# Optimization experiments

Hardware: AMD Instinct MI355X
Metric: run time of the kernel (lower is better)

## Reference

```python
import jax, jax.numpy as jnp
import numpy as np

B, D = 64, 65536   # batch, num default boxes
NEG_POS = 3        # negative:positive mining ratio (init arg)


def _bce_with_logits(x, t):
    # numerically stable elementwise BCE-with-logits (matches torch)
    return jnp.maximum(x, 0.0) - x * t + jnp.log1p(jnp.exp(-jnp.abs(x)))


def _smooth_l1(d):
    ad = jnp.abs(d)
    return jnp.where(ad < 1.0, 0.5 * d * d, ad - 0.5)


def setup_inputs() -> dict:
    key = jax.random.key(0)
    k1, k2, k3, k4 = jax.random.split(key, 4)
    loc_data = jax.random.normal(k1, (B, D, 4), dtype=jnp.float32)
    conf_data = jax.random.normal(k2, (B, D, 1), dtype=jnp.float32)
    loc_t = jax.random.normal(k3, (B, D, 4), dtype=jnp.float32)
    conf_t = (jax.random.uniform(k4, (B, D)) < 0.02).astype(jnp.int32)
    return {"loc_data": loc_data, "conf_data": conf_data,
            "loc_t": loc_t, "conf_t": conf_t}


def reference(loc_data, conf_data, loc_t, conf_t):
    pos = conf_t > 0                                  # [B, D]
    num_pos = pos.sum(axis=1, keepdims=True)          # [B, 1]

    # ---- localization loss: smooth-L1 mean over positive box coords ----
    pf = pos[:, :, None].astype(loc_data.dtype)       # [B, D, 1]
    sl1 = _smooth_l1(loc_data - loc_t) * pf           # [B, D, 4]
    n_loc_elems = pf.sum() * 4.0                      # masked-gather -> mean
    loss_l = sl1.sum() / n_loc_elems

    # ---- confidence loss with hard negative mining ----
    logits = conf_data[:, :, 0]                       # [B, D]
    bce = _bce_with_logits(logits, conf_t.astype(logits.dtype))
    bce_neg = jnp.where(pos, 0.0, bce)                # zero-out positives
    # double argsort -> per-row rank of each element's loss (descending)
    loss_idx = jnp.argsort(-bce_neg, axis=1)          # [B, D]
    idx_rank = jnp.argsort(loss_idx, axis=1)          # [B, D]
    num_neg = jnp.minimum(num_pos * NEG_POS, D)       # [B, 1]
    neg = idx_rank < num_neg                          # top-k hardest negatives
    sel = (pos | neg).astype(logits.dtype)            # [B, D]
    loss_c = (bce * sel).sum() / sel.sum()            # mean over selected

    N = num_pos.sum().astype(logits.dtype)
    return (loss_l / N, loss_c / N)
```

## Files before the change

### kernel.cpp

```cpp
#include <hip/hip_runtime.h>
#include <stdint.h>


#define B_ 64
#define D_ 65536
#define NEGPOS 3
#define BPR 16
#define NBLK (B_ * BPR)
#define CHUNK (D_ / BPR)
#define XC 1.25f
#define CAPC 16384
#define NREG 32
#define HBINS 4096
#define XRANGE 5.0f
#define CJCAP 1024

#define OFF_SL1P     0
#define OFF_BCEP     8192
#define OFF_NP       16384
#define OFF_CC       20480
#define OFF_NEGSUM   24576
#define OFF_KSEL     25088
#define OFF_CAND     32768

__device__ __forceinline__ float softplus_f(float x) {
    return fmaxf(x, 0.0f) + log1pf(expf(-fabsf(x)));
}

__device__ __forceinline__ unsigned sortkey(float x) {
    unsigned u = __float_as_uint(x);
    return (u & 0x80000000u) ? ~u : (u | 0x80000000u);
}
__device__ __forceinline__ float unsortkey(unsigned s) {
    unsigned u = (s & 0x80000000u) ? (s & 0x7FFFFFFFu) : ~s;
    return __uint_as_float(u);
}

__device__ __forceinline__ int bin_of_x(float x) {
    int b = (int)((x - XC) * ((float)HBINS / XRANGE));
    return max(0, min(HBINS - 1, b));
}

__device__ __forceinline__ float smooth_l1_4(float4 a, float4 b) {
    float s = 0.0f, d, ad;
    d = a.x - b.x; ad = fabsf(d); s += (ad < 1.0f) ? 0.5f * d * d : ad - 0.5f;
    d = a.y - b.y; ad = fabsf(d); s += (ad < 1.0f) ? 0.5f * d * d : ad - 0.5f;
    d = a.z - b.z; ad = fabsf(d); s += (ad < 1.0f) ? 0.5f * d * d : ad - 0.5f;
    d = a.w - b.w; ad = fabsf(d); s += (ad < 1.0f) ? 0.5f * d * d : ad - 0.5f;
    return s;
}

__device__ __forceinline__ double wredD(double v) {
#pragma unroll
    for (int o = 32; o > 0; o >>= 1) v += __shfl_down(v, o, 64);
    return v;
}
__device__ __forceinline__ int wredI(int v) {
#pragma unroll
    for (int o = 32; o > 0; o >>= 1) v += __shfl_down(v, o, 64);
    return v;
}

__global__ void __launch_bounds__(256)
mbl_k1(const float4* __restrict__ loc4, const float* __restrict__ conf,
       const float4* __restrict__ loct4, const int* __restrict__ conft,
       unsigned char* __restrict__ ws)
{
    __shared__ float lcand[CHUNK];
    __shared__ unsigned short lpos[CHUNK];
    __shared__ unsigned wtot[4];
    __shared__ double wr[8];

    const int block = blockIdx.x;
    const int base = block * CHUNK;
    const float4* c4 = (const float4*)(conf + base);
    const int4*   t4 = (const int4*)(conft + base);
    const int lane = threadIdx.x & 63, wid = threadIdx.x >> 6;

    float4 xv[4]; int4 tv[4];
#pragma unroll
    for (int it = 0; it < 4; it++) {
        const int g = threadIdx.x + it * 256;
        xv[it] = c4[g];
        tv[it] = t4[g];
    }

    double bcep = 0.0;
    unsigned cntc = 0, cntp = 0;
#pragma unroll
    for (int it = 0; it < 4; it++) {
#pragma unroll
        for (int c = 0; c < 4; c++) {
            float x = (c == 0) ? xv[it].x : (c == 1) ? xv[it].y : (c == 2) ? xv[it].z : xv[it].w;
            int   t = (c == 0) ? tv[it].x : (c == 1) ? tv[it].y : (c == 2) ? tv[it].z : tv[it].w;
            if (t > 0) { cntp++; bcep += (double)(softplus_f(x) - x); }
            else if (x >= XC) cntc++;
        }
    }

    unsigned pk = (cntc << 16) | cntp;
    unsigned incl = pk;
#pragma unroll
    for (int o = 1; o < 64; o <<= 1) {
        unsigned v = __shfl_up(incl, o, 64);
        if (lane >= o) incl += v;
    }
    unsigned excl = incl - pk;
    if (lane == 63) wtot[wid] = incl;
    __syncthreads();
    unsigned wbase = 0;
    for (int w = 0; w < wid; w++) wbase += wtot[w];
    const unsigned tot = wtot[0] + wtot[1] + wtot[2] + wtot[3];
    const unsigned totc = tot >> 16, totp = tot & 0xFFFFu;
    unsigned offc = (excl >> 16) + (wbase >> 16);
    unsigned offp = (excl & 0xFFFFu) + (wbase & 0xFFFFu);

#pragma unroll
    for (int it = 0; it < 4; it++) {
#pragma unroll
        for (int c = 0; c < 4; c++) {
            float x = (c == 0) ? xv[it].x : (c == 1) ? xv[it].y : (c == 2) ? xv[it].z : xv[it].w;
            int   t = (c == 0) ? tv[it].x : (c == 1) ? tv[it].y : (c == 2) ? tv[it].z : tv[it].w;
            const int li = (threadIdx.x + it * 256) * 4 + c;
            if (t > 0) lpos[offp++] = (unsigned short)li;
            else if (x >= XC) lcand[offc++] = x;
        }
    }
    __syncthreads();

    float* seg = (float*)(ws + OFF_CAND) + (size_t)block * CHUNK;
    for (unsigned i = threadIdx.x; i < totc; i += 256) seg[i] = lcand[i];

    double sl1 = 0.0;
    for (unsigned i = threadIdx.x; i < totp; i += 256) {
        const int e = base + (int)lpos[i];
        sl1 += (double)smooth_l1_4(loc4[e], loct4[e]);
    }

    double s1 = wredD(sl1), s2 = wredD(bcep);
    if (lane == 0) { wr[wid] = s1; wr[4 + wid] = s2; }
    __syncthreads();
    if (threadIdx.x == 0) {
        ((double*)(ws + OFF_SL1P))[block] = wr[0] + wr[1] + wr[2] + wr[3];
        ((double*)(ws + OFF_BCEP))[block] = wr[4] + wr[5] + wr[6] + wr[7];
        ((unsigned*)(ws + OFF_NP))[block] = totp;
        ((unsigned*)(ws + OFF_CC))[block] = totc;
    }
}

__device__ __forceinline__ int blockSumI(int v, int* sh) {
    int w = wredI(v);
    const int lane = threadIdx.x & 63, wid = threadIdx.x >> 6;
    __syncthreads();
    if (lane == 0) sh[wid] = w;
    __syncthreads();
    return sh[0] + sh[1] + sh[2] + sh[3];
}

__global__ void __launch_bounds__(256)
mbl_ksel(const float* __restrict__ conf, const int* __restrict__ conft,
         unsigned char* __restrict__ ws)
{
    __shared__ unsigned segoff[BPR + 1];
    __shared__ unsigned hist[HBINS];
    __shared__ unsigned part[256];
    __shared__ unsigned ubuf[CJCAP];
    __shared__ unsigned shJ, shRemJ, shCj, shT;
    __shared__ int shI[4];
    __shared__ double wr[4];

    const int row = blockIdx.x;
    const unsigned* cc = (const unsigned*)(ws + OFF_CC) + row * BPR;
    const unsigned* npb = (const unsigned*)(ws + OFF_NP) + row * BPR;

    if (threadIdx.x == 0) {
        unsigned o = 0;
        int np = 0;
#pragma unroll
        for (int s = 0; s < BPR; s++) { segoff[s] = o; o += cc[s]; np += (int)npb[s]; }
        segoff[BPR] = o;
        shI[0] = np;
    }
    __syncthreads();
    const int np = shI[0];
    const unsigned n = segoff[BPR];
    long long k = (long long)np * NEGPOS;
    if (k > D_) k = D_;
    long long negs = (long long)D_ - np;
    if (k > negs) k = negs;
    if (threadIdx.x == 0) ((int*)(ws + OFF_KSEL))[row] = (int)k;
    if (k <= 0) {
        if (threadIdx.x == 0) ((double*)(ws + OFF_NEGSUM))[row] = 0.0;
        return;
    }
    __syncthreads();

    const bool fb = ((long long)n < k) || (n > (unsigned)(NREG * 256)) ||
                    (n > (unsigned)CAPC);
    const float* cand = (const float*)(ws + OFF_CAND);
    const float* rowc = conf + row * D_;
    const int*   rowt = conft + row * D_;
    const int lane = threadIdx.x & 63, wid = threadIdx.x >> 6;
    unsigned Tkey;
    int rem;

    if (!fb) {
        unsigned keys[NREG];
#pragma unroll
        for (int j = 0; j < NREG; j++) {
            const unsigned g = (unsigned)(j * 256) + threadIdx.x;
            unsigned key = 0u;
            if (g < n) {
                int s = 0;
#pragma unroll
                for (int st = 8; st > 0; st >>= 1)
                    if (s + st <= BPR && segoff[s + st] <= g) s += st;
                const unsigned idx = g - segoff[s];
                key = sortkey(cand[(size_t)(row * BPR + s) * CHUNK + idx]);
            }
            keys[j] = key;
        }

        for (int i = threadIdx.x; i < HBINS; i += 256) hist[i] = 0;
        __syncthreads();
#pragma unroll
        for (int j = 0; j < NREG; j++)
            if (keys[j]) atomicAdd(&hist[bin_of_x(unsortkey(keys[j]))], 1u);
        __syncthreads();

        {
            unsigned s = 0; const int b0 = threadIdx.x * 16;
#pragma unroll
            for (int i = 0; i < 16; i++) s += hist[b0 + i];
            part[threadIdx.x] = s;
        }
        __syncthreads();
        if (threadIdx.x == 0) {
            long long cum = 0; unsigned J = 0, remJ = 0;
            for (int t = 255; t >= 0; t--) {
                if (cum + (long long)part[t] >= k) {
                    for (int b = t * 16 + 15; b >= t * 16; b--) {
                        cum += hist[b];
                        if (cum >= k) {
                            J = (unsigned)b;
                            remJ = (unsigned)(k - (cum - (long long)hist[b]));
                            break;
                        }
                    }
                    break;
                }
                cum += part[t];
            }
            shJ = J; shRemJ = remJ; shCj = 0;
        }
        __syncthreads();
        const unsigned J = shJ, remJ = shRemJ;

#pragma unroll
        for (int j = 0; j < NREG; j++) {
            if (keys[j] && (unsigned)bin_of_x(unsortkey(keys[j])) == J) {
                unsigned p = atomicAdd(&shCj, 1u);
                if (p < CJCAP) ubuf[p] = keys[j];
            }
        }
        __syncthreads();
        const unsigned cj = shCj;

        if (cj <= CJCAP) {
            for (unsigned i = threadIdx.x; i < cj; i += 256) {
                const unsigned ki = ubuf[i];
                unsigned gt = 0, ge = 0;
                for (unsigned l = 0; l < cj; l++) {
                    const unsigned kl = ubuf[l];
                    gt += (kl > ki) ? 1u : 0u;
                    ge += (kl >= ki) ? 1u : 0u;
                }
                if (gt < remJ && ge >= remJ) shT = ki;
            }
            __syncthreads();
            Tkey = shT;
        } else {
            unsigned lo = 0u, hi = 0xFFFFFFFFu;
            for (int it = 0; it < 32; it++) {
                const unsigned mid = lo + ((hi - lo) >> 1);
                int c = 0;
#pragma unroll
                for (int j = 0; j < NREG; j++) c += (keys[j] > mid) ? 1 : 0;
                const int tot = blockSumI(c, shI);
                if ((long long)tot >= k) lo = mid; else hi = mid;
            }
            Tkey = hi;
        }

        int c = 0;
        double acc = 0.0;
#pragma unroll
        for (int j = 0; j < NREG; j++) {
            if (keys[j] > Tkey) { c++; acc += (double)softplus_f(unsortkey(keys[j])); }
        }
        const int tot = blockSumI(c, shI);
        rem = (int)(k - (long long)tot);
        double t = wredD(acc);
        if (lane == 0) wr[wid] = t;
        __syncthreads();
        if (threadIdx.x == 0)
            ((double*)(ws + OFF_NEGSUM))[row] =
                wr[0] + wr[1] + wr[2] + wr[3] +
                (double)rem * (double)softplus_f(unsortkey(Tkey));
    } else {
        unsigned lo = 0u, hi = 0xFFFFFFFFu;
        for (int it = 0; it < 32; it++) {
            const unsigned mid = lo + ((hi - lo) >> 1);
            int c = 0;
            for (int i = threadIdx.x; i < D_; i += 256)
                if (rowt[i] <= 0 && sortkey(rowc[i]) > mid) c++;
            const int tot = blockSumI(c, shI);
            if ((long long)tot >= k) lo = mid; else hi = mid;
        }
        Tkey = hi;
        int c = 0;
        double acc = 0.0;
        for (int i = threadIdx.x; i < D_; i += 256) {
            if (rowt[i] <= 0) {
                float x = rowc[i];
                if (sortkey(x) > Tkey) { c++; acc += (double)softplus_f(x); }
            }
        }
        rem = (int)(k - (long long)blockSumI(c, shI));
        double t = wredD(acc);
        if (lane == 0) wr[wid] = t;
        __syncthreads();
        if (threadIdx.x == 0)
            ((double*)(ws + OFF_NEGSUM))[row] =
                wr[0] + wr[1] + wr[2] + wr[3] +
                (double)rem * (double)softplus_f(unsortkey(Tkey));
    }
}

__global__ void __launch_bounds__(256)
mbl_k5(unsigned char* __restrict__ ws, float* __restrict__ out)
{
    __shared__ double wrA[4], wrB[4], wrC[4];
    __shared__ int shN[4], shK[4];
    const double* sl1p = (const double*)(ws + OFF_SL1P);
    const double* bcep = (const double*)(ws + OFF_BCEP);
    const unsigned* npb = (const unsigned*)(ws + OFF_NP);
    const int* ksel = (const int*)(ws + OFF_KSEL);
    const double* ns = (const double*)(ws + OFF_NEGSUM);

    double a = 0.0, b = 0.0, c = 0.0;
    int n = 0, kk = 0;
    for (int i = threadIdx.x; i < NBLK; i += 256) {
        a += sl1p[i]; b += bcep[i]; n += (int)npb[i];
    }
    if (threadIdx.x < 64) { kk = ksel[threadIdx.x]; c = ns[threadIdx.x]; }

    double ra = wredD(a), rb = wredD(b), rc = wredD(c);
    int rn = wredI(n), rk = wredI(kk);
    const int lane = threadIdx.x & 63, wid = threadIdx.x >> 6;
    if (lane == 0) { wrA[wid] = ra; wrB[wid] = rb; wrC[wid] = rc; shN[wid] = rn; shK[wid] = rk; }
    __syncthreads();
    if (threadIdx.x == 0) {
        double SL1 = wrA[0] + wrA[1] + wrA[2] + wrA[3];
        double BCE = wrB[0] + wrB[1] + wrB[2] + wrB[3];
        double NSUM = wrC[0] + wrC[1] + wrC[2] + wrC[3];
        double Np = (double)(shN[0] + shN[1] + shN[2] + shN[3]);
        double Kt = (double)(shK[0] + shK[1] + shK[2] + shK[3]);
        double out0 = (Np > 0.0) ? (SL1 / (4.0 * Np)) / Np : 0.0;
        double denom = Np + Kt;
        double out1 = (Np > 0.0 && denom > 0.0) ? ((BCE + NSUM) / denom) / Np : 0.0;
        out[0] = (float)out0;
        out[1] = (float)out1;
    }
}

extern "C" void kernel_launch(void* const* d_in, const int* in_sizes, int n_in,
                              void* d_out, int out_size, void* d_ws, size_t ws_size,
                              hipStream_t stream)
{
    const float4* loc4  = (const float4*)d_in[0];
    const float*  conf  = (const float*)d_in[1];
    const float4* loct4 = (const float4*)d_in[2];
    const int*    conft = (const int*)d_in[3];
    unsigned char* ws = (unsigned char*)d_ws;
    float* out = (float*)d_out;

    mbl_k1<<<dim3(NBLK), dim3(256), 0, stream>>>(loc4, conf, loct4, conft, ws);
    mbl_ksel<<<dim3(B_), dim3(256), 0, stream>>>(conf, conft, ws);
    mbl_k5<<<dim3(1), dim3(256), 0, stream>>>(ws, out);
}
```

Baseline: 195.2 us.

## Stage candidates in LDS and parallelize histogram threshold search in ksel

The top-k selection kernel now copies each row's candidate logits into a shared-memory buffer with coalesced per-segment loads, replacing the 32 register keys per thread that needed a per-element segment binary search. The serial single-thread scan over the histogram is replaced by a wave-shuffle suffix scan, so every thread checks its own 16-bin group for the threshold bin. Threshold comparisons work on floats directly instead of converted sort keys. The goal is lower register pressure and less serial work, at the cost of 32KB more LDS, which may reduce occupancy.

```diff
diff --git a/kernel.cpp b/kernel.cpp
--- a/kernel.cpp
+++ b/kernel.cpp
@@ -9,8 +9,7 @@
 #define NBLK (B_ * BPR)
 #define CHUNK (D_ / BPR)
 #define XC 1.25f
-#define CAPC 16384
-#define NREG 32
+#define LCAP 8192
 #define HBINS 4096
 #define XRANGE 5.0f
 #define CJCAP 1024
@@ -25,15 +24,6 @@
 
 __device__ __forceinline__ float softplus_f(float x) {
     return fmaxf(x, 0.0f) + log1pf(expf(-fabsf(x)));
-}
-
-__device__ __forceinline__ unsigned sortkey(float x) {
-    unsigned u = __float_as_uint(x);
-    return (u & 0x80000000u) ? ~u : (u | 0x80000000u);
-}
-__device__ __forceinline__ float unsortkey(unsigned s) {
-    unsigned u = (s & 0x80000000u) ? (s & 0x7FFFFFFFu) : ~s;
-    return __uint_as_float(u);
 }
 
 __device__ __forceinline__ int bin_of_x(float x) {
@@ -161,28 +151,42 @@
 mbl_ksel(const float* __restrict__ conf, const int* __restrict__ conft,
          unsigned char* __restrict__ ws)
 {
-    __shared__ unsigned segoff[BPR + 1];
+    __shared__ float lval[LCAP];
     __shared__ unsigned hist[HBINS];
     __shared__ unsigned part[256];
     __shared__ unsigned ubuf[CJCAP];
-    __shared__ unsigned shJ, shRemJ, shCj, shT;
+    __shared__ unsigned segoff[BPR + 1];
+    __shared__ unsigned scc[BPR];
+    __shared__ unsigned wsuf[4];
+    __shared__ unsigned shJ, shRemJ, shCj, shNP;
+    __shared__ float shXT;
     __shared__ int shI[4];
     __shared__ double wr[4];
 
     const int row = blockIdx.x;
     const unsigned* cc = (const unsigned*)(ws + OFF_CC) + row * BPR;
     const unsigned* npb = (const unsigned*)(ws + OFF_NP) + row * BPR;
-
-    if (threadIdx.x == 0) {
-        unsigned o = 0;
-        int np = 0;
-#pragma unroll
-        for (int s = 0; s < BPR; s++) { segoff[s] = o; o += cc[s]; np += (int)npb[s]; }
-        segoff[BPR] = o;
-        shI[0] = np;
-    }
-    __syncthreads();
-    const int np = shI[0];
+    const int lane = threadIdx.x & 63, wid = threadIdx.x >> 6;
+
+    if (wid == 0) {
+        unsigned c = (lane < BPR) ? cc[lane] : 0u;
+        unsigned p = (lane < BPR) ? npb[lane] : 0u;
+        unsigned inc = c;
+#pragma unroll
+        for (int o = 1; o < BPR; o <<= 1) {
+            unsigned v = __shfl_up(inc, o, 64);
+            if (lane >= o) inc += v;
+        }
+        unsigned ptot = p;
+#pragma unroll
+        for (int o = 1; o < BPR; o <<= 1) ptot += __shfl_down(ptot, o, 64);
+        if (lane < BPR) { segoff[lane] = inc - c; scc[lane] = c; }
+        if (lane == BPR - 1) segoff[BPR] = inc;
+        if (lane == 0) { shNP = ptot; shCj = 0; }
+    }
+    __syncthreads();
+
+    const int np = (int)shNP;
     const unsigned n = segoff[BPR];
     long long k = (long long)np * NEGPOS;
     if (k > D_) k = D_;
@@ -193,39 +197,25 @@
         if (threadIdx.x == 0) ((double*)(ws + OFF_NEGSUM))[row] = 0.0;
         return;
     }
-    __syncthreads();
-
-    const bool fb = ((long long)n < k) || (n > (unsigned)(NREG * 256)) ||
-                    (n > (unsigned)CAPC);
+
     const float* cand = (const float*)(ws + OFF_CAND);
     const float* rowc = conf + row * D_;
     const int*   rowt = conft + row * D_;
-    const int lane = threadIdx.x & 63, wid = threadIdx.x >> 6;
-    unsigned Tkey;
+    const bool fb = ((long long)n < k) || (n > (unsigned)LCAP);
+    float xT;
     int rem;
 
     if (!fb) {
-        unsigned keys[NREG];
-#pragma unroll
-        for (int j = 0; j < NREG; j++) {
-            const unsigned g = (unsigned)(j * 256) + threadIdx.x;
-            unsigned key = 0u;
-            if (g < n) {
-                int s = 0;
-#pragma unroll
-                for (int st = 8; st > 0; st >>= 1)
-                    if (s + st <= BPR && segoff[s + st] <= g) s += st;
-                const unsigned idx = g - segoff[s];
-                key = sortkey(cand[(size_t)(row * BPR + s) * CHUNK + idx]);
-            }
-            keys[j] = key;
-        }
-
+        {
+            const int s = threadIdx.x >> 4, li = threadIdx.x & 15;
+            const float* gseg = cand + (size_t)(row * BPR + s) * CHUNK;
+            const unsigned cs = scc[s], d0 = segoff[s];
+            for (unsigned i = li; i < cs; i += 16) lval[d0 + i] = gseg[i];
+        }
         for (int i = threadIdx.x; i < HBINS; i += 256) hist[i] = 0;
         __syncthreads();
-#pragma unroll
-        for (int j = 0; j < NREG; j++)
-            if (keys[j]) atomicAdd(&hist[bin_of_x(unsortkey(keys[j]))], 1u);
+        for (unsigned i = threadIdx.x; i < n; i += 256)
+            atomicAdd(&hist[bin_of_x(lval[i])], 1u);
         __syncthreads();
 
         {
@@ -233,34 +223,38 @@
 #pragma unroll
             for (int i = 0; i < 16; i++) s += hist[b0 + i];
             part[threadIdx.x] = s;
-        }
-        __syncthreads();
-        if (threadIdx.x == 0) {
-            long long cum = 0; unsigned J = 0, remJ = 0;
-            for (int t = 255; t >= 0; t--) {
-                if (cum + (long long)part[t] >= k) {
-                    for (int b = t * 16 + 15; b >= t * 16; b--) {
-                        cum += hist[b];
-                        if (cum >= k) {
-                            J = (unsigned)b;
-                            remJ = (unsigned)(k - (cum - (long long)hist[b]));
-                            break;
-                        }
+            unsigned suf = s;
+#pragma unroll
+            for (int o = 1; o < 64; o <<= 1) {
+                unsigned v = __shfl_down(suf, o, 64);
+                if (lane + o < 64) suf += v;
+            }
+            if (lane == 0) wsuf[wid] = suf;
+            __syncthreads();
+            unsigned add = 0;
+            for (int w = wid + 1; w < 4; w++) add += wsuf[w];
+            suf += add;
+            const unsigned sufx = suf - s;
+            if ((long long)sufx < k && (long long)suf >= k) {
+                long long cum = sufx;
+                for (int b = threadIdx.x * 16 + 15; b >= threadIdx.x * 16; b--) {
+                    cum += hist[b];
+                    if (cum >= k) {
+                        shJ = (unsigned)b;
+                        shRemJ = (unsigned)(k - (cum - (long long)hist[b]));
+                        break;
                     }
-                    break;
                 }
-                cum += part[t];
-            }
-            shJ = J; shRemJ = remJ; shCj = 0;
+            }
         }
         __syncthreads();
         const unsigned J = shJ, remJ = shRemJ;
 
-#pragma unroll
-        for (int j = 0; j < NREG; j++) {
-            if (keys[j] && (unsigned)bin_of_x(unsortkey(keys[j])) == J) {
+        for (unsigned i = threadIdx.x; i < n; i += 256) {
+            float x = lval[i];
+            if ((unsigned)bin_of_x(x) == J) {
                 unsigned p = atomicAdd(&shCj, 1u);
-                if (p < CJCAP) ubuf[p] = keys[j];
+                if (p < CJCAP) ubuf[p] = __float_as_uint(x);
             }
         }
         __syncthreads();
@@ -268,35 +262,36 @@
 
         if (cj <= CJCAP) {
             for (unsigned i = threadIdx.x; i < cj; i += 256) {
-                const unsigned ki = ubuf[i];
+                const float xi = __uint_as_float(ubuf[i]);
                 unsigned gt = 0, ge = 0;
                 for (unsigned l = 0; l < cj; l++) {
-                    const unsigned kl = ubuf[l];
-                    gt += (kl > ki) ? 1u : 0u;
-                    ge += (kl >= ki) ? 1u : 0u;
+                    const float xl = __uint_as_float(ubuf[l]);
+                    gt += (xl > xi) ? 1u : 0u;
+                    ge += (xl >= xi) ? 1u : 0u;
                 }
-                if (gt < remJ && ge >= remJ) shT = ki;
+                if (gt < remJ && ge >= remJ) shXT = xi;
             }
             __syncthreads();
-            Tkey = shT;
+            xT = shXT;
         } else {
-            unsigned lo = 0u, hi = 0xFFFFFFFFu;
-            for (int it = 0; it < 32; it++) {
-                const unsigned mid = lo + ((hi - lo) >> 1);
+            float flo = XC - 1.0f, fhi = XC + XRANGE + 1.0f;
+            for (int it = 0; it < 40; it++) {
+                const float mid = 0.5f * (flo + fhi);
                 int c = 0;
-#pragma unroll
-                for (int j = 0; j < NREG; j++) c += (keys[j] > mid) ? 1 : 0;
+                for (unsigned i = threadIdx.x; i < n; i += 256)
+                    if (lval[i] > mid) c++;
                 const int tot = blockSumI(c, shI);
-                if ((long long)tot >= k) lo = mid; else hi = mid;
-            }
-            Tkey = hi;
+                if ((long long)tot >= k) flo = mid; else fhi = mid;
+                if (!(flo < fhi)) break;
+            }
+            xT = fhi;
         }
 
         int c = 0;
         double acc = 0.0;
-#pragma unroll
-        for (int j = 0; j < NREG; j++) {
-            if (keys[j] > Tkey) { c++; acc += (double)softplus_f(unsortkey(keys[j])); }
+        for (unsigned i = threadIdx.x; i < n; i += 256) {
+            float x = lval[i];
+            if (x > xT) { c++; acc += (double)softplus_f(x); }
         }
         const int tot = blockSumI(c, shI);
         rem = (int)(k - (long long)tot);
@@ -306,24 +301,27 @@
         if (threadIdx.x == 0)
             ((double*)(ws + OFF_NEGSUM))[row] =
                 wr[0] + wr[1] + wr[2] + wr[3] +
-                (double)rem * (double)softplus_f(unsortkey(Tkey));
+                (double)rem * (double)softplus_f(xT);
     } else {
         unsigned lo = 0u, hi = 0xFFFFFFFFu;
         for (int it = 0; it < 32; it++) {
             const unsigned mid = lo + ((hi - lo) >> 1);
+            unsigned um = (mid & 0x80000000u) ? (mid & 0x7FFFFFFFu) : ~mid;
+            float fm = __uint_as_float(um);
             int c = 0;
             for (int i = threadIdx.x; i < D_; i += 256)
-                if (rowt[i] <= 0 && sortkey(rowc[i]) > mid) c++;
+                if (rowt[i] <= 0 && rowc[i] > fm) c++;
             const int tot = blockSumI(c, shI);
             if ((long long)tot >= k) lo = mid; else hi = mid;
         }
-        Tkey = hi;
+        unsigned uT = (hi & 0x80000000u) ? (hi & 0x7FFFFFFFu) : ~hi;
+        xT = __uint_as_float(uT);
         int c = 0;
         double acc = 0.0;
         for (int i = threadIdx.x; i < D_; i += 256) {
             if (rowt[i] <= 0) {
                 float x = rowc[i];
-                if (sortkey(x) > Tkey) { c++; acc += (double)softplus_f(x); }
+                if (x > xT) { c++; acc += (double)softplus_f(x); }
             }
         }
         rem = (int)(k - (long long)blockSumI(c, shI));
@@ -333,7 +331,7 @@
         if (threadIdx.x == 0)
             ((double*)(ws + OFF_NEGSUM))[row] =
                 wr[0] + wr[1] + wr[2] + wr[3] +
-                (double)rem * (double)softplus_f(unsortkey(Tkey));
+                (double)rem * (double)softplus_f(xT);
     }
 }
 
```

New measurement: 174.8 us. 10.5% less time.
